# Optimization experiments

Measured on AMD Instinct MI355X. Metric: run time of the kernel, lower is better.

The kernel has to match this reference:

```python
import jax, jax.numpy as jnp
import numpy as np

B_, S_, F_, N_, H_ = 4, 8192, 512, 64, 2048  # batch, seq, features, state_dim, mlp hidden
EPS = 1e-5


def setup_inputs() -> dict:
    key = jax.random.key(0)
    ks = jax.random.split(key, 24)
    F, N, H = F_, N_, H_

    def nrm(k, shape, scale=1.0):
        return jax.random.normal(k, shape, dtype=jnp.float32) * scale

    inp = {}
    inp['x'] = nrm(ks[0], (B_, S_, F))
    inp['cond'] = nrm(ks[1], (B_, F))
    n = jnp.arange(N, dtype=jnp.float32)
    for i, p in enumerate(['fwd', 'bwd']):
        b = 2 + i * 6
        inp[p + '_logAre'] = jnp.log(n + 0.5)          # HiPPO-diag: A_real = -(n+0.5)
        inp[p + '_Aim'] = jnp.pi * n                    # HiPPO-diag: A_imag = pi*n
        inp[p + '_Bre'] = nrm(ks[b], (N, F), 1.0 / np.sqrt(N))
        inp[p + '_Bim'] = nrm(ks[b + 1], (N, F), 1.0 / np.sqrt(N))
        inp[p + '_Cre'] = nrm(ks[b + 2], (F, N), 1.0 / np.sqrt(F))
        inp[p + '_Cim'] = nrm(ks[b + 3], (F, N), 1.0 / np.sqrt(F))
        inp[p + '_D'] = nrm(ks[b + 4], (F,))
        inp[p + '_logdt'] = jax.random.uniform(ks[b + 5], (N,), minval=jnp.log(0.001), maxval=jnp.log(0.1))
    inp['proj_w'] = nrm(ks[14], (2 * F, F), 1.0 / np.sqrt(2 * F))
    inp['proj_b'] = jnp.zeros((F,), jnp.float32)
    # AdaLN modulation: Dense(6F) on silu(cond); zero-init in the model, small random here
    inp['ada_w'] = nrm(ks[15], (F, 6 * F), 0.02)
    inp['ada_b'] = jnp.zeros((6 * F,), jnp.float32)
    inp['mlp_w1'] = nrm(ks[16], (F, H), 1.0 / np.sqrt(F))
    inp['mlp_b1'] = jnp.zeros((H,), jnp.float32)
    inp['mlp_w2'] = nrm(ks[17], (H, F), 1.0 / np.sqrt(H))
    inp['mlp_b2'] = jnp.zeros((F,), jnp.float32)
    return inp


def _ln(x):
    mu = jnp.mean(x, axis=-1, keepdims=True)
    v = jnp.mean(jnp.square(x - mu), axis=-1, keepdims=True)
    return (x - mu) * jax.lax.rsqrt(v + EPS)


def _s5(u, logAre, Aim, Bre, Bim, Cre, Cim, D, logdt):
    dt = jnp.exp(logdt)
    A = -jnp.exp(logAre) + 1j * Aim                       # [N] complex diagonal
    A_bar = jnp.exp(A * dt)                               # ZOH discretization
    B_bar = (A_bar[:, None] - 1.0) / (A[:, None] + 1e-8) * (Bre + 1j * Bim)  # [N,F]
    u32 = u.astype(jnp.float32)
    Bu = jnp.einsum('bsf,nf->bsn', u32, B_bar)            # [B,S,N] complex
    Ab = jnp.broadcast_to(A_bar[None, None, :], Bu.shape)

    def op(e1, e2):
        a1, b1 = e1
        a2, b2 = e2
        return (a1 * a2, a2 * b1 + b2)

    _, xs = jax.lax.associative_scan(op, (Ab, Bu), axis=1)
    y = jnp.einsum('fn,bsn->bsf', Cre + 1j * Cim, xs).real + D * u32
    return y.astype(u.dtype)


def reference(x, cond, fwd_logAre, fwd_Aim, fwd_Bre, fwd_Bim, fwd_Cre, fwd_Cim, fwd_D, fwd_logdt,
              bwd_logAre, bwd_Aim, bwd_Bre, bwd_Bim, bwd_Cre, bwd_Cim, bwd_D, bwd_logdt,
              proj_w, proj_b, ada_w, ada_b, mlp_w1, mlp_b1, mlp_w2, mlp_b2):
    mods = jax.nn.silu(cond) @ ada_w + ada_b              # [B,6F]
    sh1, sc1, g1, sh2, sc2, g2 = [m[:, None, :] for m in jnp.split(mods, 6, axis=-1)]
    h = _ln(x) * (1.0 + sc1) + sh1
    y_fwd = _s5(h, fwd_logAre, fwd_Aim, fwd_Bre, fwd_Bim, fwd_Cre, fwd_Cim, fwd_D, fwd_logdt)
    y_bwd = jnp.flip(_s5(jnp.flip(h, axis=1), bwd_logAre, bwd_Aim, bwd_Bre, bwd_Bim, bwd_Cre, bwd_Cim, bwd_D, bwd_logdt), axis=1)
    y = jnp.concatenate([y_fwd, y_bwd], axis=-1) @ proj_w + proj_b
    x = x + g1 * y
    h2 = _ln(x) * (1.0 + sc2) + sh2
    x = x + g2 * (jax.nn.gelu(h2 @ mlp_w1 + mlp_b1) @ mlp_w2 + mlp_b2)
    return x
```

## Files before the change

kernel.cpp:

```cpp
#include <hip/hip_runtime.h>
#include <hip/hip_bf16.h>

typedef unsigned short u16;
typedef __attribute__((ext_vector_type(8))) short bf16x8;
typedef __attribute__((ext_vector_type(4))) float f32x4;

#define Bc 4
#define Sc 8192
#define Fc 512
#define Nc 64
#define Hc 2048
#define SIXF 3072

__device__ __forceinline__ u16 f2bf(float v) {
  __hip_bfloat16 h = __float2bfloat16(v);
  return *reinterpret_cast<u16*>(&h);
}
__device__ __forceinline__ float bf2f(u16 u) {
  return __uint_as_float(((unsigned)u) << 16);
}
__device__ __forceinline__ float ldf(const void* p, long i, int bf) {
  return bf ? bf2f(((const u16*)p)[i]) : ((const float*)p)[i];
}

__device__ __forceinline__ void ld16(const u16* g, u16* l) {
  __builtin_amdgcn_global_load_lds(
      (const __attribute__((address_space(1))) unsigned int*)g,
      (__attribute__((address_space(3))) unsigned int*)l,
      16, 0, 0);
}

__device__ __forceinline__ void xcd_swz(int& bx, int& by) {
  int gx = gridDim.x;
  int nwg = gx * gridDim.y;
  int lin = blockIdx.x + gx * blockIdx.y;
  if ((nwg & 7) == 0) {
    int q = nwg >> 3;
    lin = (lin & 7) * q + (lin >> 3);
  }
  bx = lin % gx;
  by = lin / gx;
}

__global__ void k_detect(const u16* __restrict__ x, int* __restrict__ flag) {
  if (threadIdx.x == 0) {
    int cnt = 0;
    for (int i = 0; i < 256; ++i) {
      int e = (x[i] >> 7) & 0xFF;
      cnt += (e >= 130);
    }
    *flag = (cnt >= 16) ? 0 : 1;
  }
}

__global__ void k_convert(const void* __restrict__ src, float* __restrict__ dst,
                          int n, const int* __restrict__ flag) {
  int bf = *flag;
  int i = blockIdx.x * blockDim.x + threadIdx.x;
  int stride = gridDim.x * blockDim.x;
  for (int j = i; j < n; j += stride) dst[j] = ldf(src, j, bf);
}

__global__ __launch_bounds__(256) void k_mods_init(const void* __restrict__ ada_b,
                                                   const int* __restrict__ flag,
                                                   float* __restrict__ mods) {
  int bf = *flag;
  int col = blockIdx.x * 256 + threadIdx.x;
  float v = ldf(ada_b, col, bf);
  for (int b = 0; b < Bc; ++b) mods[b * SIXF + col] = v;
}

__global__ __launch_bounds__(256) void k_mods2(const void* __restrict__ cond,
                                               const void* __restrict__ ada_w,
                                               const int* __restrict__ flag,
                                               float* __restrict__ mods) {
  int bf = *flag;
  int b = blockIdx.y;
  int f0 = blockIdx.z * 128;
  int col = blockIdx.x * 256 + threadIdx.x;
  __shared__ float sc[128];
  for (int i = threadIdx.x; i < 128; i += 256) {
    float c = ldf(cond, b * Fc + f0 + i, bf);
    sc[i] = c / (1.f + expf(-c));
  }
  __syncthreads();
  float acc = 0.f;
  for (int f = 0; f < 128; ++f) acc = fmaf(sc[f], ldf(ada_w, (long)(f0 + f) * SIXF + col, bf), acc);
  atomicAdd(&mods[b * SIXF + col], acc);
}

__global__ void k_prep(const void* lAf, const void* Aif, const void* Brf, const void* Bif, const void* ldtf,
                       const void* lAb, const void* Aib, const void* Brb, const void* Bib, const void* ldtb,
                       const int* __restrict__ flag,
                       u16* __restrict__ Wbup, float* __restrict__ Abar) {
  int bf = *flag;
  int dir = blockIdx.x;
  int f0 = blockIdx.y * 64;
  int n = threadIdx.x;
  const void* lA = dir ? lAb : lAf;
  const void* Ai = dir ? Aib : Aif;
  const void* Br = dir ? Brb : Brf;
  const void* Bi = dir ? Bib : Bif;
  const void* ld = dir ? ldtb : ldtf;
  float dt  = expf(ldf(ld, n, bf));
  float Are = -expf(ldf(lA, n, bf));
  float Aim = ldf(Ai, n, bf);
  float er  = expf(Are * dt);
  float abr = er * cosf(Aim * dt);
  float abi = er * sinf(Aim * dt);
  if (blockIdx.y == 0) {
    Abar[(dir * Nc + n) * 2 + 0] = abr;
    Abar[(dir * Nc + n) * 2 + 1] = abi;
  }
  float dr = Are + 1e-8f, di = Aim;
  float den = dr * dr + di * di;
  float nr = abr - 1.f, ni = abi;
  float cr = (nr * dr + ni * di) / den;
  float ci = (ni * dr - nr * di) / den;
  int col_re = dir * 128 + n, col_im = dir * 128 + 64 + n;
  for (int f = f0; f < f0 + 64; ++f) {
    float br = ldf(Br, n * Fc + f, bf), bi = ldf(Bi, n * Fc + f, bf);
    Wbup[(((f >> 3) * 256) + col_re) * 8 + (f & 7)] = f2bf(cr * br - ci * bi);
    Wbup[(((f >> 3) * 256) + col_im) * 8 + (f & 7)] = f2bf(cr * bi + ci * br);
  }
}

__global__ __launch_bounds__(256) void k_P2p(const void* Df, const void* Db, const void* pw,
                                             const int* __restrict__ flag, u16* __restrict__ Wyp) {
  int bf = *flag;
  int idx = blockIdx.x * 256 + threadIdx.x;
  int f1 = idx >> 9, fo = idx & 511;
  float v = ldf(Df, f1, bf) * ldf(pw, (long)f1 * Fc + fo, bf) +
            ldf(Db, f1, bf) * ldf(pw, (long)(Fc + f1) * Fc + fo, bf);
  Wyp[((((f1 >> 3) + 64) * Fc) + fo) * 8 + (f1 & 7)] = f2bf(v);
}

__global__ __launch_bounds__(256) void k_Cpm(const void* Cref, const void* Cimf,
                                             const void* Creb, const void* Cimb,
                                             const int* __restrict__ flag, u16* __restrict__ Cpm) {
  int bf = *flag;
  int k = blockIdx.x;
  int dir = k >> 7, c = (k >> 6) & 1, n = k & 63;
  const void* C = dir ? (c ? Cimb : Creb) : (c ? Cimf : Cref);
  float sgn = c ? -1.f : 1.f;
  for (int f = threadIdx.x; f < Fc; f += 256)
    Cpm[k * Fc + f] = f2bf(sgn * ldf(C, (long)f * Nc + n, bf));
}

__global__ __launch_bounds__(256) void k_Wpack(const void* __restrict__ src, const int* __restrict__ flag,
                                               int log2N, u16* __restrict__ dst) {
  int bf = *flag;
  long i = (long)blockIdx.x * 256 + threadIdx.x;
  int Nn = 1 << log2N;
  long k8 = i >> log2N;
  int n = (int)(i & (Nn - 1));
  u16 tmp[8];
#pragma unroll
  for (int j = 0; j < 8; ++j)
    tmp[j] = f2bf(ldf(src, ((k8 << 3) + j) * (long)Nn + n, bf));
  *(ushort4*)(dst + i * 8)     = *(ushort4*)tmp;
  *(ushort4*)(dst + i * 8 + 4) = *(ushort4*)(tmp + 4);
}

__global__ __launch_bounds__(256) void k_ln(const void* __restrict__ src, int srcmode,
                                            long src_tok_base, int b0,
                                            const int* __restrict__ flag,
                                            const float* __restrict__ mods,
                                            int sh_base, int sc_base,
                                            u16* __restrict__ dst, int ldd, int dcol) {
  int bf = srcmode ? 1 : *flag;
  long lt = blockIdx.x;
  int b = b0 + (int)(lt >> 13);
  int t = threadIdx.x;
  long si = (src_tok_base + lt) * Fc;
  float x0 = ldf(src, si + t, bf);
  float x1 = ldf(src, si + t + 256, bf);
  float s = x0 + x1, qq = x0 * x0 + x1 * x1;
  for (int o = 32; o; o >>= 1) { s += __shfl_down(s, o); qq += __shfl_down(qq, o); }
  __shared__ float ss[4], sq[4];
  int w = t >> 6;
  if ((t & 63) == 0) { ss[w] = s; sq[w] = qq; }
  __syncthreads();
  float S = ss[0] + ss[1] + ss[2] + ss[3];
  float Q = sq[0] + sq[1] + sq[2] + sq[3];
  float mu = S * (1.f / Fc);
  float var = Q * (1.f / Fc) - mu * mu;
  float rs = rsqrtf(var + 1e-5f);
  const float* mb = mods + b * SIXF;
  float h0 = (x0 - mu) * rs * (1.f + mb[sc_base + t]) + mb[sh_base + t];
  float h1 = (x1 - mu) * rs * (1.f + mb[sc_base + t + 256]) + mb[sh_base + t + 256];
  dst[lt * (long)ldd + dcol + t] = f2bf(h0);
  dst[lt * (long)ldd + dcol + t + 256] = f2bf(h1);
}

struct SmemA { u16 As[2][128 * 64]; u16 Ws[2][64 * 128]; };

__device__ __forceinline__ void mfma_gemm128(SmemA& sm, const u16* __restrict__ A, long row0,
                                             int lda, int K,
                                             const u16* __restrict__ Wp, int N, int col0,
                                             f32x4 (&acc)[4][4]) {
  const int tid = threadIdx.x;
  const int l = tid & 63, q = l >> 4, li = l & 15;
  const int w = tid >> 6;
  const int wm = (w >> 1) << 6, wn = (w & 1) << 6;
  const int m0 = tid >> 3;
  const int kc0 = (tid & 7) ^ (m0 & 7);
  const long aoff0 = (row0 + m0) * (long)lda + (kc0 << 3);
  const long woff0 = (long)(tid >> 7) * ((long)N << 3) + ((long)(col0 + (tid & 127)) << 3);
  const int lb = w << 9;
  const int T = K >> 6;
  int cur = 0;
  auto stage = [&](int buf, int k0) {
#pragma unroll
    for (int it = 0; it < 4; ++it)
      ld16(A + aoff0 + (long)it * ((long)lda << 5) + k0, sm.As[buf] + (it << 11) + lb);
#pragma unroll
    for (int it = 0; it < 4; ++it)
      ld16(Wp + woff0 + (long)k0 * N + (long)it * ((long)N << 4), sm.Ws[buf] + (it << 11) + lb);
  };
  stage(0, 0);
  for (int t = 0; t < T; ++t) {
    if (t + 1 < T) {
      stage(cur ^ 1, (t + 1) << 6);
      asm volatile("s_waitcnt vmcnt(8)" ::: "memory");
    } else {
      asm volatile("s_waitcnt vmcnt(0)" ::: "memory");
    }
    __builtin_amdgcn_s_barrier();
    __builtin_amdgcn_sched_barrier(0);
    const u16* As = sm.As[cur];
    const u16* Ws = sm.Ws[cur];
#pragma unroll
    for (int ks = 0; ks < 2; ++ks) {
      bf16x8 af[4], bw[4];
#pragma unroll
      for (int mt = 0; mt < 4; ++mt) {
        int mrow = wm + (mt << 4) + li;
        af[mt] = *(const bf16x8*)(As + (((mrow << 3) + (((ks << 2) + q) ^ (mrow & 7))) << 3));
      }
#pragma unroll
      for (int nt = 0; nt < 4; ++nt) {
        int n = wn + (nt << 4) + li;
        bw[nt] = *(const bf16x8*)(Ws + (((((ks << 2) + q) << 7) | n) << 3));
      }
#pragma unroll
      for (int mt = 0; mt < 4; ++mt)
#pragma unroll
        for (int nt = 0; nt < 4; ++nt)
          acc[mt][nt] = __builtin_amdgcn_mfma_f32_16x16x32_bf16(af[mt], bw[nt], acc[mt][nt], 0, 0, 0);
    }
    __builtin_amdgcn_s_barrier();
    __builtin_amdgcn_sched_barrier(0);
    cur ^= 1;
  }
}

struct SmemB { u16 As[2][256 * 64]; u16 Ws[2][64 * 256]; };

__device__ __forceinline__ void mfma_gemm256(SmemB& sm, const u16* __restrict__ A, long row0,
                                             int lda, int K,
                                             const u16* __restrict__ Wp, int N, int col0,
                                             f32x4 (&acc)[8][4]) {
  const int tid = threadIdx.x;
  const int l = tid & 63, q = l >> 4, li = l & 15;
  const int w = tid >> 6;
  const int wm = (w >> 2) << 7, wn = (w & 3) << 6;
  const int m0 = tid >> 3;
  const int kc0 = (tid & 7) ^ (m0 & 7);
  const long aoff0 = (row0 + m0) * (long)lda + (kc0 << 3);
  const long woff0 = (long)(tid >> 8) * ((long)N << 3) + ((long)(col0 + (tid & 255)) << 3);
  const int lb = w << 9;
  const int T = K >> 6;
  int cur = 0;
  auto stage = [&](int buf, int k0) {
#pragma unroll
    for (int it = 0; it < 4; ++it)
      ld16(A + aoff0 + (long)it * ((long)lda << 6) + k0, sm.As[buf] + (it << 12) + lb);
#pragma unroll
    for (int it = 0; it < 4; ++it)
      ld16(Wp + woff0 + (long)k0 * N + (long)it * ((long)N << 4), sm.Ws[buf] + (it << 12) + lb);
  };
  stage(0, 0);
  for (int t = 0; t < T; ++t) {
    if (t + 1 < T) {
      stage(cur ^ 1, (t + 1) << 6);
      asm volatile("s_waitcnt vmcnt(8)" ::: "memory");
    } else {
      asm volatile("s_waitcnt vmcnt(0)" ::: "memory");
    }
    __builtin_amdgcn_s_barrier();
    __builtin_amdgcn_sched_barrier(0);
    const u16* As = sm.As[cur];
    const u16* Ws = sm.Ws[cur];
    __builtin_amdgcn_s_setprio(1);
#pragma unroll
    for (int ks = 0; ks < 2; ++ks) {
      bf16x8 bw[4];
#pragma unroll
      for (int nt = 0; nt < 4; ++nt) {
        int n = wn + (nt << 4) + li;
        bw[nt] = *(const bf16x8*)(Ws + (((((ks << 2) + q) << 8) | n) << 3));
      }
#pragma unroll
      for (int mt = 0; mt < 8; ++mt) {
        int mrow = wm + (mt << 4) + li;
        bf16x8 af = *(const bf16x8*)(As + (((mrow << 3) + (((ks << 2) + q) ^ (mrow & 7))) << 3));
#pragma unroll
        for (int nt = 0; nt < 4; ++nt)
          acc[mt][nt] = __builtin_amdgcn_mfma_f32_16x16x32_bf16(af, bw[nt], acc[mt][nt], 0, 0, 0);
      }
    }
    __builtin_amdgcn_s_setprio(0);
    __builtin_amdgcn_s_barrier();
    __builtin_amdgcn_sched_barrier(0);
    cur ^= 1;
  }
}

__global__ __launch_bounds__(256) void k_Gp2(const u16* __restrict__ Cpm, const u16* __restrict__ pwp,
                                             u16* __restrict__ Wyp) {
  __shared__ SmemA sm;
  f32x4 acc[4][4] = {};
  int bx, by; xcd_swz(bx, by);
  long row0 = (long)by * 128;
  int col0 = bx << 7;
  int dir = (int)(row0 >> 7);
  mfma_gemm128(sm, Cpm, row0, Fc, Fc, pwp + (size_t)dir * 262144, Fc, col0, acc);
  const int l = threadIdx.x & 63, q = l >> 4, li = l & 15;
  const int w = threadIdx.x >> 6;
  const int wm = (w >> 1) << 6, wn = (w & 1) << 6;
#pragma unroll
  for (int mt = 0; mt < 4; ++mt)
#pragma unroll
    for (int nt = 0; nt < 4; ++nt)
#pragma unroll
      for (int r = 0; r < 4; ++r) {
        int k = (int)row0 + wm + (mt << 4) + (q << 2) + r;
        int col = col0 + wn + (nt << 4) + li;
        u16 v = f2bf(acc[mt][nt][r]);
        size_t i0 = (((size_t)(k >> 3)) * Fc + col) * 8 + (k & 7);
        Wyp[i0] = v;
        Wyp[i0 + (size_t)32 * Fc * 8] = v;
      }
}

__global__ __launch_bounds__(256) void k_gemm_bu(const u16* __restrict__ hp,
                                                 const u16* __restrict__ Wbup,
                                                 int nb, float* __restrict__ Bu) {
  __shared__ SmemA sm;
  f32x4 acc[4][4] = {};
  int bx, by; xcd_swz(bx, by);
  long row0 = (long)by * 128;
  int col0 = bx << 7;
  mfma_gemm128(sm, hp, row0, 1024, Fc, Wbup, 256, col0, acc);
  const int l = threadIdx.x & 63, q = l >> 4, li = l & 15;
  const int w = threadIdx.x >> 6;
  const int wm = (w >> 1) << 6, wn = (w & 1) << 6;
#pragma unroll
  for (int mt = 0; mt < 4; ++mt) {
#pragma unroll
    for (int nt = 0; nt < 4; ++nt) {
      int col = col0 + wn + (nt << 4) + li;
      int dir = col >> 7, cc = (col >> 6) & 1, n = col & 63;
#pragma unroll
      for (int r = 0; r < 4; ++r) {
        long lt = row0 + wm + (mt << 4) + (q << 2) + r;
        int lb = (int)(lt >> 13), s = (int)(lt & 8191);
        int spos = dir ? (Sc - 1 - s) : s;
        Bu[((((long)dir * nb + lb) * Nc + n) * Sc + spos) * 2 + cc] = acc[mt][nt][r];
      }
    }
  }
}

__global__ __launch_bounds__(256) void k_scan(float* __restrict__ Bu, const float* __restrict__ Abar,
                                              int nb) {
  int blk = blockIdx.x;
  int per_dir = nb * 64;
  int dir = blk / per_dir;
  int rem = blk - dir * per_dir;
  int lb = rem >> 6, n = rem & 63;
  float ar = Abar[(dir * Nc + n) * 2 + 0];
  float ai = Abar[(dir * Nc + n) * 2 + 1];
  float* base = Bu + (((long)dir * nb + lb) * Nc + n) * Sc * 2;
  int t = threadIdx.x;
  float4 loc[16];
  float lr = 0.f, li = 0.f;
  const float4* bp = (const float4*)base + t * 16;
#pragma unroll
  for (int j = 0; j < 16; ++j) {
    float4 v = bp[j];
    loc[j] = v;
    float nr = fmaf(ar, lr, fmaf(-ai, li, v.x));
    float ni = fmaf(ar, li, fmaf(ai, lr, v.y));
    lr = fmaf(ar, nr, fmaf(-ai, ni, v.z));
    li = fmaf(ar, ni, fmaf(ai, nr, v.w));
  }
  __shared__ float sr[256], si[256];
  float pr = ar, pi = ai;
  for (int k = 0; k < 5; ++k) { float t2 = pr * pr - pi * pi; pi = 2.f * pr * pi; pr = t2; }
  float vr = lr, vi = li;
  for (int step = 1; step < 256; step <<= 1) {
    sr[t] = vr; si[t] = vi;
    __syncthreads();
    if (t >= step) {
      float orr = sr[t - step], oii = si[t - step];
      vr = vr + pr * orr - pi * oii;
      vi = vi + pr * oii + pi * orr;
    }
    __syncthreads();
    float t2 = pr * pr - pi * pi; pi = 2.f * pr * pi; pr = t2;
  }
  sr[t] = vr; si[t] = vi;
  __syncthreads();
  float xr = (t == 0) ? 0.f : sr[t - 1];
  float xi = (t == 0) ? 0.f : si[t - 1];
  float4* op = (float4*)base + t * 16;
#pragma unroll
  for (int j = 0; j < 16; ++j) {
    float4 v = loc[j];
    float nr = fmaf(ar, xr, fmaf(-ai, xi, v.x));
    float ni = fmaf(ar, xi, fmaf(ai, xr, v.y));
    xr = fmaf(ar, nr, fmaf(-ai, ni, v.z));
    xi = fmaf(ar, ni, fmaf(ai, nr, v.w));
    float4 o; o.x = nr; o.y = ni; o.z = xr; o.w = xi;
    op[j] = o;
  }
}

__global__ __launch_bounds__(256) void k_xs_t(const float* __restrict__ xs, int nb,
                                              u16* __restrict__ hxl) {
  __shared__ float tile[32 * 257];
  long t0 = (long)blockIdx.x * 32;
  int lb = (int)(t0 >> 13);
  int s0 = (int)(t0 & 8191);
  int tid = threadIdx.x;
  int ls = tid & 31;
  int half = (tid >> 5) & 1;
  int wv = tid >> 6;
#pragma unroll 4
  for (int cg = 0; cg < 32; ++cg) {
    int col = cg * 8 + wv * 2 + half;
    int dir = col >> 7, cc = (col >> 6) & 1, n = col & 63;
    int spos = dir ? (Sc - 1 - (s0 + ls)) : (s0 + ls);
    float v = xs[((((long)dir * nb + lb) * Nc + n) * Sc + spos) * 2 + cc];
    tile[ls * 257 + col] = v;
  }
  __syncthreads();
  for (int j = 0; j < 32; ++j) {
    float v = tile[j * 257 + tid];
    u16 hi = f2bf(v);
    long lt = t0 + j;
    hxl[lt * 1024 + tid] = hi;
    hxl[lt * 1024 + 256 + tid] = f2bf(v - bf2f(hi));
  }
}

__global__ __launch_bounds__(512, 2) void k_gemm_y(const u16* __restrict__ hxl,
                                                   const u16* __restrict__ Wyp,
                                                   const void* __restrict__ xraw, long tok_base, int b0,
                                                   const int* __restrict__ flag,
                                                   const float* __restrict__ mods,
                                                   const float* __restrict__ pb,
                                                   u16* __restrict__ out1) {
  __shared__ SmemB sm;
  f32x4 acc[8][4] = {};
  int bx, by; xcd_swz(bx, by);
  long row0 = (long)by << 8;
  int col0 = bx << 8;
  mfma_gemm256(sm, hxl, row0, 1024, 1024, Wyp, Fc, col0, acc);
  int bf = *flag;
  const int l = threadIdx.x & 63, q = l >> 4, li = l & 15;
  const int w = threadIdx.x >> 6;
  const int wm = (w >> 2) << 7, wn = (w & 3) << 6;
#pragma unroll
  for (int mt = 0; mt < 8; ++mt) {
#pragma unroll
    for (int r = 0; r < 4; ++r) {
      long lt = row0 + wm + (mt << 4) + (q << 2) + r;
      int b = b0 + (int)(lt >> 13);
      const float* mb = mods + b * SIXF + 2 * Fc;
#pragma unroll
      for (int nt = 0; nt < 4; ++nt) {
        int col = col0 + wn + (nt << 4) + li;
        float xv = ldf(xraw, (tok_base + lt) * Fc + col, bf);
        out1[lt * Fc + col] = f2bf(xv + mb[col] * (acc[mt][nt][r] + pb[col]));
      }
    }
  }
}

__device__ __forceinline__ float gelu_t(float u) {
  float z = 0.7978845608028654f * fmaf(0.044715f * u * u, u, u);
  float e = __builtin_amdgcn_exp2f(z * -2.8853900817779268f);
  return u * __builtin_amdgcn_rcpf(1.f + e);
}

__global__ __launch_bounds__(512, 2) void k_mlp1(const u16* __restrict__ h2, const u16* __restrict__ W1p,
                                                 const float* __restrict__ b1, long crow0,
                                                 u16* __restrict__ tbuf) {
  __shared__ SmemB sm;
  f32x4 acc[8][4] = {};
  int bx, by; xcd_swz(bx, by);
  long row0 = crow0 + ((long)by << 8);
  int col0 = bx << 8;
  mfma_gemm256(sm, h2, row0, Fc, Fc, W1p, Hc, col0, acc);
  const int l = threadIdx.x & 63, q = l >> 4, li = l & 15;
  const int w = threadIdx.x >> 6;
  const int wm = (w >> 2) << 7, wn = (w & 3) << 6;
#pragma unroll
  for (int mt = 0; mt < 8; ++mt) {
#pragma unroll
    for (int r = 0; r < 4; ++r) {
      long lr2 = row0 - crow0 + wm + (mt << 4) + (q << 2) + r;
#pragma unroll
      for (int nt = 0; nt < 4; ++nt) {
        int col = col0 + wn + (nt << 4) + li;
        tbuf[lr2 * Hc + col] = f2bf(gelu_t(acc[mt][nt][r] + b1[col]));
      }
    }
  }
}

__global__ __launch_bounds__(256) void k_mlp2(const u16* __restrict__ tbuf, const u16* __restrict__ W2p,
                                              const float* __restrict__ b2, const u16* __restrict__ out1,
                                              const float* __restrict__ mods, long crow0,
                                              long tok_base, int b0,
                                              const int* __restrict__ flag, void* __restrict__ dout) {
  __shared__ SmemA sm;
  f32x4 acc[4][4] = {};
  int bx, by; xcd_swz(bx, by);
  long lrow0 = (long)by * 128;
  int col0 = bx << 7;
  mfma_gemm128(sm, tbuf, lrow0, Hc, Hc, W2p, Fc, col0, acc);
  int bf = *flag;
  const int l = threadIdx.x & 63, q = l >> 4, li = l & 15;
  const int w = threadIdx.x >> 6;
  const int wm = (w >> 1) << 6, wn = (w & 1) << 6;
#pragma unroll
  for (int mt = 0; mt < 4; ++mt) {
#pragma unroll
    for (int r = 0; r < 4; ++r) {
      long lt = crow0 + lrow0 + wm + (mt << 4) + (q << 2) + r;
      int b = b0 + (int)(lt >> 13);
      const float* mb = mods + b * SIXF + 5 * Fc;
#pragma unroll
      for (int nt = 0; nt < 4; ++nt) {
        int col = col0 + wn + (nt << 4) + li;
        float v = bf2f(out1[lt * Fc + col]) + mb[col] * (acc[mt][nt][r] + b2[col]);
        long oi = (tok_base + lt) * Fc + col;
        if (bf) ((u16*)dout)[oi] = f2bf(v);
        else    ((float*)dout)[oi] = v;
      }
    }
  }
}

extern "C" void kernel_launch(void* const* d_in, const int* in_sizes, int n_in,
                              void* d_out, int out_size, void* d_ws, size_t ws_size,
                              hipStream_t stream) {
  char* ws = (char*)d_ws;
  size_t off = 0;
  auto alloc = [&](size_t bytes) -> char* {
    char* p = ws + off;
    off += (bytes + 255) & ~(size_t)255;
    return p;
  };
  int*   flag = (int*)  alloc(4);
  float* mods = (float*)alloc((size_t)Bc * SIXF * 4);
  float* Abar = (float*)alloc(2 * Nc * 2 * 4);
  float* pbf  = (float*)alloc(Fc * 4);
  float* b1f  = (float*)alloc(Hc * 4);
  float* b2f  = (float*)alloc(Fc * 4);
  u16* Wbup = (u16*)alloc((size_t)Fc * 256 * 2);
  u16* Wyp  = (u16*)alloc((size_t)128 * Fc * 8 * 2);
  u16* W1p  = (u16*)alloc((size_t)Fc * Hc * 2);
  u16* W2p  = (u16*)alloc((size_t)Hc * Fc * 2);
  u16* pwp  = (u16*)alloc((size_t)1024 * Fc * 2);
  u16* Cpm  = (u16*)alloc((size_t)256 * Fc * 2);
  size_t off_static = off;

  const size_t U = (size_t)Sc * Fc * 2;
  int nb = 4;
  while (nb > 1 && off_static + (size_t)nb * 4 * U + 4096 > ws_size) nb >>= 1;

  u16*   hxl  = (u16*)  alloc((size_t)nb * U * 2);
  float* Bu   = (float*)alloc((size_t)nb * U);
  u16*   out1 = (u16*)  alloc((size_t)nb * U);
  u16* tch = hxl;
  u16* h2  = (u16*)Bu;

  k_detect<<<1, 64, 0, stream>>>((const u16*)d_in[0], flag);
  k_convert<<<2, 256, 0, stream>>>(d_in[19], pbf, Fc, flag);
  k_convert<<<8, 256, 0, stream>>>(d_in[23], b1f, Hc, flag);
  k_convert<<<2, 256, 0, stream>>>(d_in[25], b2f, Fc, flag);
  k_mods_init<<<12, 256, 0, stream>>>(d_in[21], flag, mods);
  k_mods2<<<dim3(12, Bc, 4), 256, 0, stream>>>(d_in[1], d_in[20], flag, mods);
  k_prep<<<dim3(2, 8), 64, 0, stream>>>(d_in[2], d_in[3], d_in[4], d_in[5], d_in[9],
                                        d_in[10], d_in[11], d_in[12], d_in[13], d_in[17],
                                        flag, Wbup, Abar);
  k_P2p<<<(Fc * Fc) / 256, 256, 0, stream>>>(d_in[8], d_in[16], d_in[18], flag, Wyp);
  k_Wpack<<<256, 256, 0, stream>>>(d_in[18], flag, 9, pwp);
  k_Cpm<<<256, 256, 0, stream>>>(d_in[6], d_in[7], d_in[14], d_in[15], flag, Cpm);
  k_Gp2<<<dim3(4, 2), 256, 0, stream>>>(Cpm, pwp, Wyp);
  k_Wpack<<<512, 256, 0, stream>>>(d_in[22], flag, 11, W1p);
  k_Wpack<<<512, 256, 0, stream>>>(d_in[24], flag, 9, W2p);

  for (int b0 = 0; b0 < Bc; b0 += nb) {
    long tok_base = (long)b0 * Sc;
    long rows = (long)nb * Sc;
    k_ln<<<rows, 256, 0, stream>>>(d_in[0], 0, tok_base, b0, flag, mods, 0, Fc, hxl, 1024, 512);
    k_gemm_bu<<<dim3(2, rows / 128), 256, 0, stream>>>(hxl + 512, Wbup, nb, Bu);
    k_scan<<<2 * nb * 64, 256, 0, stream>>>(Bu, Abar, nb);
    k_xs_t<<<rows / 32, 256, 0, stream>>>(Bu, nb, hxl);
    k_gemm_y<<<dim3(2, rows / 256), 512, 0, stream>>>(hxl, Wyp, d_in[0], tok_base, b0,
                                                      flag, mods, pbf, out1);
    k_ln<<<rows, 256, 0, stream>>>(out1, 1, 0, b0, flag, mods, 3 * Fc, 4 * Fc, h2, 512, 0);
    long RC = rows / 2;
    for (int ch = 0; ch < 2; ++ch) {
      long crow0 = ch * RC;
      k_mlp1<<<dim3(8, RC / 256), 512, 0, stream>>>(h2, W1p, b1f, crow0, tch);
      k_mlp2<<<dim3(4, RC / 128), 256, 0, stream>>>(tch, W2p, b2f, out1, mods, crow0,
                                                    tok_base, b0, flag, d_out);
    }
  }
  (void)n_in; (void)out_size; (void)in_sizes;
}
```

Before: 623.5 us.

## Deepen 256-tile GEMM pipeline to four stages with half-size K slices

Replaces the double-buffered 64-wide K staging in the 256x256 MFMA GEMM with a four-buffer ring of 32-wide K slices, keeping three loads in flight and adjusting vmcnt waits and the LDS swizzle to match. Total LDS footprint stays the same. The aim is to hide global-memory latency better in k_gemm_y and k_mlp1. In exchange there are twice as many barriers per K, and the new swizzle may cause different LDS bank behaviour.

```diff
diff --git a/kernel.cpp b/kernel.cpp
--- a/kernel.cpp
+++ b/kernel.cpp
@@ -255,9 +255,9 @@
   }
 }
 
-struct SmemB { u16 As[2][256 * 64]; u16 Ws[2][64 * 256]; };
-
-__device__ __forceinline__ void mfma_gemm256(SmemB& sm, const u16* __restrict__ A, long row0,
+struct SmemC { u16 As[4][256 * 32]; u16 Ws[4][32 * 256]; };
+
+__device__ __forceinline__ void mfma_gemm256(SmemC& sm, const u16* __restrict__ A, long row0,
                                              int lda, int K,
                                              const u16* __restrict__ Wp, int N, int col0,
                                              f32x4 (&acc)[8][4]) {
@@ -265,55 +265,51 @@
   const int l = tid & 63, q = l >> 4, li = l & 15;
   const int w = tid >> 6;
   const int wm = (w >> 2) << 7, wn = (w & 3) << 6;
-  const int m0 = tid >> 3;
-  const int kc0 = (tid & 7) ^ (m0 & 7);
+  const int m0 = tid >> 2;
+  const int kc0 = (tid & 3) ^ ((tid >> 3) & 3);
   const long aoff0 = (row0 + m0) * (long)lda + (kc0 << 3);
   const long woff0 = (long)(tid >> 8) * ((long)N << 3) + ((long)(col0 + (tid & 255)) << 3);
-  const int lb = w << 9;
-  const int T = K >> 6;
-  int cur = 0;
-  auto stage = [&](int buf, int k0) {
-#pragma unroll
-    for (int it = 0; it < 4; ++it)
-      ld16(A + aoff0 + (long)it * ((long)lda << 6) + k0, sm.As[buf] + (it << 12) + lb);
-#pragma unroll
-    for (int it = 0; it < 4; ++it)
-      ld16(Wp + woff0 + (long)k0 * N + (long)it * ((long)N << 4), sm.Ws[buf] + (it << 12) + lb);
+  const int T = K >> 5;
+  auto stage = [&](int buf, int t) {
+    const int k0 = t << 5;
+#pragma unroll
+    for (int it = 0; it < 2; ++it)
+      ld16(A + aoff0 + (long)(it << 7) * lda + k0, sm.As[buf] + (((it << 9) + tid) << 3));
+#pragma unroll
+    for (int it = 0; it < 2; ++it)
+      ld16(Wp + woff0 + (((long)((k0 >> 3) + (it << 1)) * N) << 3),
+           sm.Ws[buf] + (((it << 9) + tid) << 3));
   };
-  stage(0, 0);
+  stage(0, 0); stage(1, 1); stage(2, 2);
   for (int t = 0; t < T; ++t) {
-    if (t + 1 < T) {
-      stage(cur ^ 1, (t + 1) << 6);
-      asm volatile("s_waitcnt vmcnt(8)" ::: "memory");
-    } else {
-      asm volatile("s_waitcnt vmcnt(0)" ::: "memory");
-    }
+    if (t + 3 < T) stage((t + 3) & 3, t + 3);
+    int rem = T - 1 - t;
+    if (rem >= 3)      asm volatile("s_waitcnt vmcnt(12)" ::: "memory");
+    else if (rem == 2) asm volatile("s_waitcnt vmcnt(8)" ::: "memory");
+    else if (rem == 1) asm volatile("s_waitcnt vmcnt(4)" ::: "memory");
+    else               asm volatile("s_waitcnt vmcnt(0)" ::: "memory");
     __builtin_amdgcn_s_barrier();
     __builtin_amdgcn_sched_barrier(0);
-    const u16* As = sm.As[cur];
-    const u16* Ws = sm.Ws[cur];
+    const u16* As = sm.As[t & 3];
+    const u16* Ws = sm.Ws[t & 3];
     __builtin_amdgcn_s_setprio(1);
-#pragma unroll
-    for (int ks = 0; ks < 2; ++ks) {
-      bf16x8 bw[4];
-#pragma unroll
-      for (int nt = 0; nt < 4; ++nt) {
-        int n = wn + (nt << 4) + li;
-        bw[nt] = *(const bf16x8*)(Ws + (((((ks << 2) + q) << 8) | n) << 3));
-      }
-#pragma unroll
-      for (int mt = 0; mt < 8; ++mt) {
-        int mrow = wm + (mt << 4) + li;
-        bf16x8 af = *(const bf16x8*)(As + (((mrow << 3) + (((ks << 2) + q) ^ (mrow & 7))) << 3));
-#pragma unroll
-        for (int nt = 0; nt < 4; ++nt)
-          acc[mt][nt] = __builtin_amdgcn_mfma_f32_16x16x32_bf16(af, bw[nt], acc[mt][nt], 0, 0, 0);
-      }
+    bf16x8 bw[4];
+#pragma unroll
+    for (int nt = 0; nt < 4; ++nt) {
+      int n = wn + (nt << 4) + li;
+      bw[nt] = *(const bf16x8*)(Ws + (((q << 8) | n) << 3));
+    }
+#pragma unroll
+    for (int mt = 0; mt < 8; ++mt) {
+      int mrow = wm + (mt << 4) + li;
+      bf16x8 af = *(const bf16x8*)(As + (((mrow << 2) + (q ^ ((mrow >> 1) & 3))) << 3));
+#pragma unroll
+      for (int nt = 0; nt < 4; ++nt)
+        acc[mt][nt] = __builtin_amdgcn_mfma_f32_16x16x32_bf16(af, bw[nt], acc[mt][nt], 0, 0, 0);
     }
     __builtin_amdgcn_s_setprio(0);
     __builtin_amdgcn_s_barrier();
     __builtin_amdgcn_sched_barrier(0);
-    cur ^= 1;
   }
 }
 
@@ -463,7 +459,7 @@
                                                    const float* __restrict__ mods,
                                                    const float* __restrict__ pb,
                                                    u16* __restrict__ out1) {
-  __shared__ SmemB sm;
+  __shared__ SmemC sm;
   f32x4 acc[8][4] = {};
   int bx, by; xcd_swz(bx, by);
   long row0 = (long)by << 8;
@@ -499,7 +495,7 @@
 __global__ __launch_bounds__(512, 2) void k_mlp1(const u16* __restrict__ h2, const u16* __restrict__ W1p,
                                                  const float* __restrict__ b1, long crow0,
                                                  u16* __restrict__ tbuf) {
-  __shared__ SmemB sm;
+  __shared__ SmemC sm;
   f32x4 acc[8][4] = {};
   int bx, by; xcd_swz(bx, by);
   long row0 = crow0 + ((long)by << 8);
```

Measured after the change: 621.6 us. About the same (-0.3%).
